# Kernel tuning notes

Measured on AMD Instinct MI355X. Metric: run time of the kernel, lower is better.

## Reference

```python
import jax, jax.numpy as jnp
import numpy as np

S, B, D_IN, D_H, D_OUT = 32, 1024, 784, 1024, 10


def setup_inputs() -> dict:
    key = jax.random.key(0)
    ks = jax.random.split(key, 8)
    inp = {
        "x": jax.random.normal(ks[0], (B, D_IN), dtype=jnp.float32),
        # variational means / log-variances (init like the torch module)
        "wm0": jax.random.normal(ks[1], (D_IN, D_H), dtype=jnp.float32) * 0.1,
        "wv0": jnp.full((D_IN, D_H), -6.0, dtype=jnp.float32),
        "bm0": jnp.full((D_H,), 0.1, dtype=jnp.float32),
        "bv0": jnp.full((D_H,), -6.0, dtype=jnp.float32),
        "wm1": jax.random.normal(ks[2], (D_H, D_H), dtype=jnp.float32) * 0.1,
        "wv1": jnp.full((D_H, D_H), -6.0, dtype=jnp.float32),
        "bm1": jnp.full((D_H,), 0.1, dtype=jnp.float32),
        "bv1": jnp.full((D_H,), -6.0, dtype=jnp.float32),
        "wlm": jax.random.normal(ks[3], (D_H, D_OUT), dtype=jnp.float32) * 0.1,
        "wlv": jnp.full((D_H, D_OUT), -6.0, dtype=jnp.float32),
        "blm": jnp.full((D_OUT,), 0.1, dtype=jnp.float32),
        "blv": jnp.full((D_OUT,), -6.0, dtype=jnp.float32),
        # reparameterization noise (torch.randn in _predict), made explicit
        "we0": jax.random.normal(ks[4], (S, D_IN, D_H), dtype=jnp.float32),
        "be0": jax.random.normal(ks[5], (S, 1, D_H), dtype=jnp.float32),
        "we1": jax.random.normal(ks[6], (S, D_H, D_H), dtype=jnp.float32),
        "be1": jax.random.normal(ks[7], (S, 1, D_H), dtype=jnp.float32),
        "wel": jax.random.normal(jax.random.fold_in(key, 100), (S, D_H, D_OUT), dtype=jnp.float32),
        "bel": jax.random.normal(jax.random.fold_in(key, 101), (S, 1, D_OUT), dtype=jnp.float32),
    }
    return inp


def reference(x, wm0, wv0, bm0, bv0, wm1, wv1, bm1, bv1,
              wlm, wlv, blm, blv, we0, be0, we1, be1, wel, bel):
    n_samples = we0.shape[0]
    # activations: (S, B, D)
    act = jnp.broadcast_to(x[None], (n_samples,) + x.shape)
    for wm, wv, bm, bv, we, be in ((wm0, wv0, bm0, bv0, we0, be0),
                                   (wm1, wv1, bm1, bv1, we1, be1)):
        W = we * jnp.exp(0.5 * wv) + wm          # (S, in, out) sampled weights
        b = be * jnp.exp(0.5 * bv) + bm          # (S, 1, out) sampled biases
        act = jax.nn.relu(jnp.einsum('sbi,sio->sbo', act, W) + b)
    # last layer: torch does (act[...,None] * W[:,None]).sum(2) == batched matmul
    Wl = wel * jnp.exp(0.5 * wlv) + wlm
    bl = bel * jnp.exp(0.5 * blv) + blm
    logits = jnp.einsum('sbi,sio->sbo', act, Wl) + bl  # (S, B, D_OUT)
    return logits
```

## Files before the change

### kernel.cpp

```cpp
#include <hip/hip_runtime.h>

typedef unsigned short u16;
typedef __bf16 bf16x8 __attribute__((ext_vector_type(8)));
typedef float f32x4 __attribute__((ext_vector_type(4)));
typedef u16 u16x8 __attribute__((ext_vector_type(8)));

__device__ __forceinline__ u16 f2bf(float f) {
  unsigned u = __builtin_bit_cast(unsigned, f);
  return (u16)((u + 0x7fffu + ((u >> 16) & 1u)) >> 16);
}

__device__ __forceinline__ void async_load16(const void* g, void* l) {
  __builtin_amdgcn_global_load_lds((const __attribute__((address_space(1))) void*)g,
                                   (__attribute__((address_space(3))) void*)l,
                                   16, 0, 0);
}

__global__ void pad_x_k(const float* __restrict__ x, u16* __restrict__ xbf) {
  int idx = blockIdx.x * 256 + threadIdx.x;
  int m = idx / 800, k = idx - m * 800;
  float v = (k < 784) ? x[m * 784 + k] : 0.f;
  xbf[idx] = f2bf(v);
}

__global__ __launch_bounds__(256) void sample_wt_k(
    const float* __restrict__ we,
    const float* __restrict__ wm,
    const float* __restrict__ wv,
    u16* __restrict__ wt,
    int K, int KB, int SC) {
  const int N = 1024;
  const int b = blockIdx.x;
  int s, kb, nb;
  if (SC >= 8) {
    int g = b & 7, r = b >> 3, spq = SC >> 3;
    int sq = r % spq, r2 = r / spq;
    nb = r2 & 3; kb = r2 >> 2;
    s = g + sq * 8;
  } else {
    s = b % SC; int r = b / SC; nb = r & 3; kb = r >> 2;
  }
  const int t = threadIdx.x;
  const int n = nb * 256 + t;
  const int kbase = kb * 32;
  const float* we_s = we + (size_t)s * K * N;

  u16 pk[32];
#pragma unroll
  for (int jo = 0; jo < 4; ++jo) {
    float v[8];
#pragma unroll
    for (int j = 0; j < 8; ++j) {
      int k = kbase + jo * 8 + j;
      v[j] = 0.f;
      if (k < K) {
        size_t idx = (size_t)k * N + n;
        v[j] = fmaf(__expf(0.5f * wv[idx]), we_s[idx], wm[idx]);
      }
    }
#pragma unroll
    for (int j = 0; j < 8; ++j) pk[jo * 8 + j] = f2bf(v[j]);
  }
  u16* dst = wt + ((size_t)s * KB + kb) * ((size_t)N * 32) + (size_t)n * 32;
#pragma unroll
  for (int q = 0; q < 4; ++q)
    *(u16x8*)(dst + q * 8) = *(const u16x8*)(pk + q * 8);
}

__global__ void sample_wl_k(const float* __restrict__ wel,
                            const float* __restrict__ wlm,
                            const float* __restrict__ wlv,
                            u16* __restrict__ wlt) {
  int idx = blockIdx.x * 256 + threadIdx.x;
  int k = idx & 1023;
  int n = (idx >> 10) & 15;
  int s = idx >> 14;
  float v = 0.f;
  if (n < 10) {
    size_t i2 = ((size_t)s * 1024 + k) * 10 + n;
    size_t iw = (size_t)k * 10 + n;
    v = fmaf(__expf(0.5f * wlv[iw]), wel[i2], wlm[iw]);
  }
  wlt[idx] = f2bf(v);
}

__global__ __launch_bounds__(256) void gemm_bt_relu(
    const u16* __restrict__ A, size_t strideAs, int ldA,
    const u16* __restrict__ Bt,
    u16* __restrict__ C,
    int Kp,
    const float* __restrict__ bm, const float* __restrict__ bv,
    const float* __restrict__ be, int s_off, int SC) {
  __shared__ __align__(16) u16 As[128 * 32];
  __shared__ __align__(16) u16 Bs[128 * 32];

  const int b = blockIdx.x;
  int sc, tile;
  if (SC >= 8) { sc = (b & 7) + ((b >> 9) << 3); tile = (b >> 3) & 63; }
  else         { sc = b >> 6; tile = b & 63; }
  const int sg = sc + s_off;
  const u16* A_s = A + (size_t)sc * strideAs;
  const u16* B_s = Bt + (size_t)sc * (size_t)1024 * Kp;
  u16* C_s = C + (size_t)sc * (size_t)1024 * 1024;

  const int m0 = (tile >> 3) * 128;
  const int n0 = (tile & 7) * 128;
  const int t = threadIdx.x;
  const int w = t >> 6, l = t & 63;
  const int quad = l >> 4, lane16 = l & 15;
  const int wm_ = (w >> 1) * 64, wn_ = (w & 1) * 64;

  f32x4 acc[4][4];
#pragma unroll
  for (int i = 0; i < 4; ++i)
#pragma unroll
    for (int j = 0; j < 4; ++j) acc[i][j] = (f32x4){0.f, 0.f, 0.f, 0.f};

  for (int k0 = 0; k0 < Kp; k0 += 32) {
    const u16* Bk = B_s + (size_t)(k0 >> 5) * (1024 * 32);
    __syncthreads();
#pragma unroll
    for (int i = 0; i < 2; ++i) {
      int p = w * 128 + i * 64 + l;
      const u16* srcA = A_s + (size_t)(m0 + (p >> 2)) * ldA + k0 + (p & 3) * 8;
      async_load16(srcA, &As[(size_t)(w * 128 + i * 64) * 8]);
      const u16* srcB = Bk + (size_t)(n0 + (p >> 2)) * 32 + (p & 3) * 8;
      async_load16(srcB, &Bs[(size_t)(w * 128 + i * 64) * 8]);
    }
    __syncthreads();

    bf16x8 af[4], bfr[4];
#pragma unroll
    for (int mi = 0; mi < 4; ++mi)
      af[mi] = *(const bf16x8*)&As[(wm_ + mi * 16 + lane16) * 32 + quad * 8];
#pragma unroll
    for (int ni = 0; ni < 4; ++ni)
      bfr[ni] = *(const bf16x8*)&Bs[(wn_ + ni * 16 + lane16) * 32 + quad * 8];
#pragma unroll
    for (int mi = 0; mi < 4; ++mi)
#pragma unroll
      for (int ni = 0; ni < 4; ++ni)
        acc[mi][ni] =
            __builtin_amdgcn_mfma_f32_16x16x32_bf16(af[mi], bfr[ni], acc[mi][ni], 0, 0, 0);
  }

#pragma unroll
  for (int ni = 0; ni < 4; ++ni) {
    int n = n0 + wn_ + ni * 16 + lane16;
    float bias = fmaf(__expf(0.5f * bv[n]), be[(size_t)sg * 1024 + n], bm[n]);
#pragma unroll
    for (int mi = 0; mi < 4; ++mi) {
#pragma unroll
      for (int r = 0; r < 4; ++r) {
        int m = m0 + wm_ + mi * 16 + quad * 4 + r;
        float v = acc[mi][ni][r] + bias;
        v = fmaxf(v, 0.f);
        C_s[(size_t)m * 1024 + n] = f2bf(v);
      }
    }
  }
}

__global__ __launch_bounds__(256) void gemm_last_k(
    const u16* __restrict__ act2, const u16* __restrict__ Wlt,
    float* __restrict__ out,
    const float* __restrict__ blm, const float* __restrict__ blv,
    const float* __restrict__ bel, int s_off) {
  __shared__ f32x4 red[4][64];
  const int b = blockIdx.x;
  const int sc = b >> 6, tile = b & 63;
  const int t = threadIdx.x;
  const int w = t >> 6, l = t & 63;
  const int quad = l >> 4, lane16 = l & 15;
  const int m0 = tile * 16;

  const u16* A_s = act2 + (size_t)sc * 1024 * 1024;
  const u16* B_s = Wlt + (size_t)sc * 16 * 1024;

  f32x4 acc = (f32x4){0.f, 0.f, 0.f, 0.f};
  const int kbase = w * 256;
#pragma unroll
  for (int k0 = 0; k0 < 256; k0 += 32) {
    int k = kbase + k0;
    bf16x8 a = *(const bf16x8*)&A_s[(size_t)(m0 + lane16) * 1024 + k + quad * 8];
    bf16x8 bb = *(const bf16x8*)&B_s[(size_t)lane16 * 1024 + k + quad * 8];
    acc = __builtin_amdgcn_mfma_f32_16x16x32_bf16(a, bb, acc, 0, 0, 0);
  }
  red[w][l] = acc;
  __syncthreads();
  if (w == 0) {
    f32x4 r = red[0][l];
#pragma unroll
    for (int ww = 1; ww < 4; ++ww) {
      f32x4 o = red[ww][l];
      r[0] += o[0]; r[1] += o[1]; r[2] += o[2]; r[3] += o[3];
    }
    int n = lane16;
    if (n < 10) {
      int sg = sc + s_off;
      float bias = fmaf(__expf(0.5f * blv[n]), bel[sg * 10 + n], blm[n]);
#pragma unroll
      for (int rr = 0; rr < 4; ++rr) {
        int m = m0 + quad * 4 + rr;
        out[((size_t)sg * 1024 + m) * 10 + n] = r[rr] + bias;
      }
    }
  }
}

extern "C" void kernel_launch(void* const* d_in, const int* in_sizes, int n_in,
                              void* d_out, int out_size, void* d_ws, size_t ws_size,
                              hipStream_t stream) {
  const float* x   = (const float*)d_in[0];
  const float* wm0 = (const float*)d_in[1];
  const float* wv0 = (const float*)d_in[2];
  const float* bm0 = (const float*)d_in[3];
  const float* bv0 = (const float*)d_in[4];
  const float* wm1 = (const float*)d_in[5];
  const float* wv1 = (const float*)d_in[6];
  const float* bm1 = (const float*)d_in[7];
  const float* bv1 = (const float*)d_in[8];
  const float* wlm = (const float*)d_in[9];
  const float* wlv = (const float*)d_in[10];
  const float* blm = (const float*)d_in[11];
  const float* blv = (const float*)d_in[12];
  const float* we0 = (const float*)d_in[13];
  const float* be0 = (const float*)d_in[14];
  const float* we1 = (const float*)d_in[15];
  const float* be1 = (const float*)d_in[16];
  const float* wel = (const float*)d_in[17];
  const float* bel = (const float*)d_in[18];
  float* out = (float*)d_out;

  const size_t sz_x    = (size_t)1024 * 800 * 2;
  const size_t sz_W0t  = (size_t)1024 * 800 * 2;
  const size_t sz_act  = (size_t)1024 * 1024 * 2;
  const size_t sz_Wlt  = (size_t)16 * 1024 * 2;
  const size_t per_s = sz_W0t + 3 * sz_act + sz_Wlt;

  int SC = 32;
  while (SC > 1 && sz_x + (size_t)SC * per_s + 4096 > ws_size) SC >>= 1;

  char* ws = (char*)d_ws;
  size_t off = 0;
  auto take = [&](size_t bsz) {
    char* p = ws + off;
    off = (off + bsz + 255) & ~(size_t)255;
    return p;
  };
  u16* xbf  = (u16*)take(sz_x);
  u16* W0t  = (u16*)take((size_t)SC * sz_W0t);
  u16* act1 = (u16*)take((size_t)SC * sz_act);
  u16* W1t  = (u16*)take((size_t)SC * sz_act);
  u16* act2 = (u16*)take((size_t)SC * sz_act);
  u16* Wlt  = (u16*)take((size_t)SC * sz_Wlt);

  pad_x_k<<<3200, 256, 0, stream>>>(x, xbf);

  const int KB0 = 25;
  const int KB1 = 32;

  for (int s0 = 0; s0 < 32; s0 += SC) {
    sample_wt_k<<<SC * KB0 * 4, 256, 0, stream>>>(
        we0 + (size_t)s0 * 784 * 1024, wm0, wv0, W0t, 784, KB0, SC);
    gemm_bt_relu<<<64 * SC, 256, 0, stream>>>(
        xbf, (size_t)0, 800, W0t, act1, 800, bm0, bv0, be0, s0, SC);
    sample_wt_k<<<SC * KB1 * 4, 256, 0, stream>>>(
        we1 + (size_t)s0 * 1024 * 1024, wm1, wv1, W1t, 1024, KB1, SC);
    gemm_bt_relu<<<64 * SC, 256, 0, stream>>>(
        act1, (size_t)1024 * 1024, 1024, W1t, act2, 1024, bm1, bv1, be1, s0, SC);
    sample_wl_k<<<SC * 64, 256, 0, stream>>>(
        wel + (size_t)s0 * 1024 * 10, wlm, wlv, Wlt);
    gemm_last_k<<<64 * SC, 256, 0, stream>>>(
        act2, Wlt, out, blm, blv, bel, s0);
  }
}
```

Measured before the change: 574.8 us.

## Rewrite batched GEMM with 256x256 tiles, BK=64, LDS double buffering and swizzle

The per-sample bf16 GEMM moves from 128x128 tiles with BK=32 and one LDS buffer to 256x256 tiles with 512 threads, BK=64, and two LDS buffers filled by async global-to-LDS loads. The loads are software-pipelined with explicit vmcnt waits, and LDS reads use an XOR swizzle to avoid bank conflicts. The weight layout is regrouped into 64-wide K blocks, and the input padding goes from 800 to 832 so K divides by 64. This aims to raise arithmetic intensity and hide load latency, at the cost of 128 KB of LDS per block, more accumulator registers, and fewer blocks (16 per sample).

```diff
diff --git a/kernel.cpp b/kernel.cpp
--- a/kernel.cpp
+++ b/kernel.cpp
@@ -18,7 +18,7 @@
 
 __global__ void pad_x_k(const float* __restrict__ x, u16* __restrict__ xbf) {
   int idx = blockIdx.x * 256 + threadIdx.x;
-  int m = idx / 800, k = idx - m * 800;
+  int m = idx / 832, k = idx - m * 832;
   float v = (k < 784) ? x[m * 784 + k] : 0.f;
   xbf[idx] = f2bf(v);
 }
@@ -43,6 +43,7 @@
   const int t = threadIdx.x;
   const int n = nb * 256 + t;
   const int kbase = kb * 32;
+  const int KB64 = (KB + 1) >> 1;
   const float* we_s = we + (size_t)s * K * N;
 
   u16 pk[32];
@@ -61,7 +62,7 @@
 #pragma unroll
     for (int j = 0; j < 8; ++j) pk[jo * 8 + j] = f2bf(v[j]);
   }
-  u16* dst = wt + ((size_t)s * KB + kb) * ((size_t)N * 32) + (size_t)n * 32;
+  u16* dst = wt + (((size_t)s * KB64 + (kb >> 1)) * 1024 + n) * 64 + (kb & 1) * 32;
 #pragma unroll
   for (int q = 0; q < 4; ++q)
     *(u16x8*)(dst + q * 8) = *(const u16x8*)(pk + q * 8);
@@ -84,78 +85,121 @@
   wlt[idx] = f2bf(v);
 }
 
-__global__ __launch_bounds__(256) void gemm_bt_relu(
+__global__ __launch_bounds__(512, 2) void gemm_bt_relu(
     const u16* __restrict__ A, size_t strideAs, int ldA,
     const u16* __restrict__ Bt,
     u16* __restrict__ C,
     int Kp,
     const float* __restrict__ bm, const float* __restrict__ bv,
     const float* __restrict__ be, int s_off, int SC) {
-  __shared__ __align__(16) u16 As[128 * 32];
-  __shared__ __align__(16) u16 Bs[128 * 32];
+  __shared__ __align__(16) u16 lds[65536];
 
   const int b = blockIdx.x;
   int sc, tile;
-  if (SC >= 8) { sc = (b & 7) + ((b >> 9) << 3); tile = (b >> 3) & 63; }
-  else         { sc = b >> 6; tile = b & 63; }
+  if (SC >= 8) { int g = b & 7, r = b >> 3; tile = r & 15; sc = g + ((r >> 4) << 3); }
+  else         { sc = b >> 4; tile = b & 15; }
   const int sg = sc + s_off;
   const u16* A_s = A + (size_t)sc * strideAs;
   const u16* B_s = Bt + (size_t)sc * (size_t)1024 * Kp;
   u16* C_s = C + (size_t)sc * (size_t)1024 * 1024;
-
-  const int m0 = (tile >> 3) * 128;
-  const int n0 = (tile & 7) * 128;
+  const int m0 = (tile >> 2) * 256;
+  const int n0 = (tile & 3) * 256;
   const int t = threadIdx.x;
-  const int w = t >> 6, l = t & 63;
-  const int quad = l >> 4, lane16 = l & 15;
-  const int wm_ = (w >> 1) * 64, wn_ = (w & 1) * 64;
-
-  f32x4 acc[4][4];
-#pragma unroll
-  for (int i = 0; i < 4; ++i)
+  const int wid = t >> 6, lane = t & 63;
+  const int quad = lane >> 4, lane16 = lane & 15;
+  const int wm2 = wid >> 2, wn4 = wid & 3;
+  const int NT = Kp >> 6;
+
+  auto stage = [&](int kt, int buf) {
+    const int k0 = kt * 64;
+#pragma unroll
+    for (int r = 0; r < 4; ++r) {
+      int c = r * 512 + t;
+      int cl = c ^ ((c >> 3) & 7);
+      const u16* srcA = A_s + (size_t)(m0 + (cl >> 3)) * ldA + k0 + (cl & 7) * 8;
+      async_load16(srcA, &lds[buf * 16384 + (r * 512 + wid * 64) * 8]);
+    }
+    const u16* Bk = B_s + (size_t)kt * (1024 * 64);
+#pragma unroll
+    for (int r = 0; r < 4; ++r) {
+      int c = r * 512 + t;
+      int cl = c ^ ((c >> 3) & 7);
+      const u16* srcB = Bk + (size_t)(n0 + (cl >> 3)) * 64 + (cl & 7) * 8;
+      async_load16(srcB, &lds[32768 + buf * 16384 + (r * 512 + wid * 64) * 8]);
+    }
+  };
+
+  auto rdA = [&](int buf, int mi, int ks) -> bf16x8 {
+    int o = (wm2 * 128 + mi * 16 + lane16) * 128 + ks * 64 + quad * 16;
+    o ^= ((o >> 7) & 7) << 4;
+    return *(const bf16x8*)((const char*)&lds[buf * 16384] + o);
+  };
+  auto rdB = [&](int buf, int ni, int ks) -> bf16x8 {
+    int o = (wn4 * 64 + ni * 16 + lane16) * 128 + ks * 64 + quad * 16;
+    o ^= ((o >> 7) & 7) << 4;
+    return *(const bf16x8*)((const char*)&lds[32768 + buf * 16384] + o);
+  };
+
+  f32x4 acc[8][4];
+#pragma unroll
+  for (int i = 0; i < 8; ++i)
 #pragma unroll
     for (int j = 0; j < 4; ++j) acc[i][j] = (f32x4){0.f, 0.f, 0.f, 0.f};
 
-  for (int k0 = 0; k0 < Kp; k0 += 32) {
-    const u16* Bk = B_s + (size_t)(k0 >> 5) * (1024 * 32);
-    __syncthreads();
-#pragma unroll
-    for (int i = 0; i < 2; ++i) {
-      int p = w * 128 + i * 64 + l;
-      const u16* srcA = A_s + (size_t)(m0 + (p >> 2)) * ldA + k0 + (p & 3) * 8;
-      async_load16(srcA, &As[(size_t)(w * 128 + i * 64) * 8]);
-      const u16* srcB = Bk + (size_t)(n0 + (p >> 2)) * 32 + (p & 3) * 8;
-      async_load16(srcB, &Bs[(size_t)(w * 128 + i * 64) * 8]);
-    }
-    __syncthreads();
-
-    bf16x8 af[4], bfr[4];
-#pragma unroll
-    for (int mi = 0; mi < 4; ++mi)
-      af[mi] = *(const bf16x8*)&As[(wm_ + mi * 16 + lane16) * 32 + quad * 8];
-#pragma unroll
-    for (int ni = 0; ni < 4; ++ni)
-      bfr[ni] = *(const bf16x8*)&Bs[(wn_ + ni * 16 + lane16) * 32 + quad * 8];
-#pragma unroll
-    for (int mi = 0; mi < 4; ++mi)
-#pragma unroll
-      for (int ni = 0; ni < 4; ++ni)
-        acc[mi][ni] =
-            __builtin_amdgcn_mfma_f32_16x16x32_bf16(af[mi], bfr[ni], acc[mi][ni], 0, 0, 0);
+  stage(0, 0);
+  stage(1, 1);
+  asm volatile("s_waitcnt vmcnt(8)" ::: "memory");
+  __builtin_amdgcn_s_barrier();
+
+  for (int T = 0; T < NT; ++T) {
+    const int cur = T & 1;
+    bf16x8 af[4], bb[4];
+#pragma unroll
+    for (int ks = 0; ks < 2; ++ks) {
+#pragma unroll
+      for (int i = 0; i < 4; ++i) bb[i] = rdB(cur, i, ks);
+#pragma unroll
+      for (int i = 0; i < 4; ++i) af[i] = rdA(cur, i, ks);
+      __builtin_amdgcn_s_setprio(1);
+#pragma unroll
+      for (int mi = 0; mi < 4; ++mi)
+#pragma unroll
+        for (int ni = 0; ni < 4; ++ni)
+          acc[mi][ni] =
+              __builtin_amdgcn_mfma_f32_16x16x32_bf16(af[mi], bb[ni], acc[mi][ni], 0, 0, 0);
+      __builtin_amdgcn_s_setprio(0);
+#pragma unroll
+      for (int i = 0; i < 4; ++i) af[i] = rdA(cur, 4 + i, ks);
+      __builtin_amdgcn_s_setprio(1);
+#pragma unroll
+      for (int mi = 0; mi < 4; ++mi)
+#pragma unroll
+        for (int ni = 0; ni < 4; ++ni)
+          acc[4 + mi][ni] =
+              __builtin_amdgcn_mfma_f32_16x16x32_bf16(af[mi], bb[ni], acc[4 + mi][ni], 0, 0, 0);
+      __builtin_amdgcn_s_setprio(0);
+    }
+    __builtin_amdgcn_sched_barrier(0);
+    __builtin_amdgcn_s_barrier();
+    if (T + 2 < NT) stage(T + 2, cur);
+    if (T + 1 < NT) {
+      if (T + 2 < NT) asm volatile("s_waitcnt vmcnt(8)" ::: "memory");
+      else            asm volatile("s_waitcnt vmcnt(0)" ::: "memory");
+      __builtin_amdgcn_s_barrier();
+      __builtin_amdgcn_sched_barrier(0);
+    }
   }
 
 #pragma unroll
   for (int ni = 0; ni < 4; ++ni) {
-    int n = n0 + wn_ + ni * 16 + lane16;
+    int n = n0 + wn4 * 64 + ni * 16 + lane16;
     float bias = fmaf(__expf(0.5f * bv[n]), be[(size_t)sg * 1024 + n], bm[n]);
 #pragma unroll
-    for (int mi = 0; mi < 4; ++mi) {
+    for (int mi = 0; mi < 8; ++mi) {
 #pragma unroll
       for (int r = 0; r < 4; ++r) {
-        int m = m0 + wm_ + mi * 16 + quad * 4 + r;
-        float v = acc[mi][ni][r] + bias;
-        v = fmaxf(v, 0.f);
-        C_s[(size_t)m * 1024 + n] = f2bf(v);
+        int m = m0 + wm2 * 128 + mi * 16 + quad * 4 + r;
+        C_s[(size_t)m * 1024 + n] = f2bf(fmaxf(acc[mi][ni][r] + bias, 0.f));
       }
     }
   }
@@ -232,8 +276,8 @@
   const float* bel = (const float*)d_in[18];
   float* out = (float*)d_out;
 
-  const size_t sz_x    = (size_t)1024 * 800 * 2;
-  const size_t sz_W0t  = (size_t)1024 * 800 * 2;
+  const size_t sz_x    = (size_t)1024 * 832 * 2;
+  const size_t sz_W0t  = (size_t)1024 * 832 * 2;
   const size_t sz_act  = (size_t)1024 * 1024 * 2;
   const size_t sz_Wlt  = (size_t)16 * 1024 * 2;
   const size_t per_s = sz_W0t + 3 * sz_act + sz_Wlt;
@@ -255,19 +299,19 @@
   u16* act2 = (u16*)take((size_t)SC * sz_act);
   u16* Wlt  = (u16*)take((size_t)SC * sz_Wlt);
 
-  pad_x_k<<<3200, 256, 0, stream>>>(x, xbf);
-
-  const int KB0 = 25;
+  pad_x_k<<<3328, 256, 0, stream>>>(x, xbf);
+
+  const int KB0 = 26;
   const int KB1 = 32;
 
   for (int s0 = 0; s0 < 32; s0 += SC) {
     sample_wt_k<<<SC * KB0 * 4, 256, 0, stream>>>(
         we0 + (size_t)s0 * 784 * 1024, wm0, wv0, W0t, 784, KB0, SC);
-    gemm_bt_relu<<<64 * SC, 256, 0, stream>>>(
-        xbf, (size_t)0, 800, W0t, act1, 800, bm0, bv0, be0, s0, SC);
+    gemm_bt_relu<<<16 * SC, 512, 0, stream>>>(
+        xbf, (size_t)0, 832, W0t, act1, 832, bm0, bv0, be0, s0, SC);
     sample_wt_k<<<SC * KB1 * 4, 256, 0, stream>>>(
         we1 + (size_t)s0 * 1024 * 1024, wm1, wv1, W1t, 1024, KB1, SC);
-    gemm_bt_relu<<<64 * SC, 256, 0, stream>>>(
+    gemm_bt_relu<<<16 * SC, 512, 0, stream>>>(
         act1, (size_t)1024 * 1024, 1024, W1t, act2, 1024, bm1, bv1, be1, s0, SC);
     sample_wl_k<<<SC * 64, 256, 0, stream>>>(
         wel + (size_t)s0 * 1024 * 10, wlm, wlv, Wlt);
```

Result: no change. 575.6 us (+0.1%).
